# Optimization experiments

Measured on AMD Instinct MI355X. Metric: run time of the kernel, lower is better.

## Reference

```python
import jax, jax.numpy as jnp
import numpy as np

H = 256; B = 64; MAXF = 32; L = 50; S = 50
TAU = 1.0; BIAS = 0.0  # m_tau / m_bias (undefined in source; fixed constants)


def setup_inputs() -> dict:
    key = jax.random.key(0)
    ks = jax.random.split(key, 16)
    s = 1.0 / np.sqrt(H)
    return {
        "self_x": jax.random.normal(ks[0], (B, H), jnp.float32),
        "common_x": jax.random.normal(ks[1], (B, MAXF, S, H), jnp.float32),
        "common_time": jax.random.uniform(ks[2], (B, MAXF, S), jnp.float32),
        "friend_x": jax.random.normal(ks[3], (B, MAXF, L, H), jnp.float32),
        "Wih0": jax.random.normal(ks[4], (3 * H, H), jnp.float32) * s,
        "Whh0": jax.random.normal(ks[5], (3 * H, H), jnp.float32) * s,
        "bih0": jax.random.normal(ks[6], (3 * H,), jnp.float32) * s,
        "bhh0": jax.random.normal(ks[7], (3 * H,), jnp.float32) * s,
        "Wih1": jax.random.normal(ks[8], (3 * H, H), jnp.float32) * s,
        "Whh1": jax.random.normal(ks[9], (3 * H, H), jnp.float32) * s,
        "bih1": jax.random.normal(ks[10], (3 * H,), jnp.float32) * s,
        "bhh1": jax.random.normal(ks[11], (3 * H,), jnp.float32) * s,
        "Wf": jax.random.normal(ks[12], (H, 2 * H), jnp.float32) * s,   # m_linear_friend
        "Wb": jax.random.normal(ks[13], (H, H), jnp.float32) * s,       # m_linear_beta
        "friend_len": jax.random.randint(ks[14], (B, MAXF), 1, L + 1, jnp.int32),
        "friend_num": jax.random.randint(ks[15], (B,), 1, MAXF + 1, jnp.int32),
        "common_len": jax.random.randint(jax.random.fold_in(key, 99), (B, MAXF), 1, S + 1, jnp.int32),
    }


def _gru_layer(x, Wih, Whh, bih, bhh):
    # x: [N, L, H] -> outputs [N, L, H]; torch GRU gate math, zero init hidden
    def step(h, xt):
        gi = xt @ Wih.T + bih
        gh = h @ Whh.T + bhh
        ir, iz, inn = jnp.split(gi, 3, axis=-1)
        hr, hz, hn = jnp.split(gh, 3, axis=-1)
        r = jax.nn.sigmoid(ir + hr)
        z = jax.nn.sigmoid(iz + hz)
        n = jnp.tanh(inn + r * hn)
        h = (1.0 - z) * n + z * h
        return h, h
    h0 = jnp.zeros((x.shape[0], Whh.shape[1]), x.dtype)
    _, ys = jax.lax.scan(step, h0, jnp.swapaxes(x, 0, 1))
    return jnp.swapaxes(ys, 0, 1)


def reference(self_x, common_x, common_time, friend_x,
              Wih0, Whh0, bih0, bhh0, Wih1, Whh1, bih1, bhh1,
              Wf, Wb, friend_len, friend_num, common_len):
    # --- GRU over all (user, friend) sequences, flattened ---
    fx = friend_x.reshape(B * MAXF, L, H)
    fx = _gru_layer(fx, Wih0, Whh0, bih0, bhh0)
    fx = _gru_layer(fx, Wih1, Whh1, bih1, bhh1)
    fx = fx.reshape(B, MAXF, L, H)

    # mask invalid time steps, gather last valid hidden state per friend
    t_mask = (jnp.arange(L)[None, None, :] < friend_len[:, :, None])  # [B,MAXF,L]
    fx = fx * t_mask[..., None].astype(fx.dtype)
    last_idx = jnp.clip(friend_len - 1, 0, L - 1)
    friend_last = jnp.take_along_axis(fx, last_idx[:, :, None, None], axis=2)[:, :, 0, :]  # [B,MAXF,H]

    # repeat_interleave(self_x) equivalent in dense layout, concat, project
    self_rep = jnp.broadcast_to(self_x[:, None, :], (B, MAXF, H))
    sf = jnp.concatenate([self_rep, friend_last], axis=-1)  # [B,MAXF,2H]
    sf = jnp.einsum('bfk,hk->bfh', sf, Wf)                   # m_linear_friend

    # attention scores over common items: bmm + softplus
    proj_c = jnp.einsum('bfsh,gh->bfsg', common_x, Wb)       # m_linear_beta, g==H
    scores = jax.nn.softplus(jnp.einsum('bfsh,bfh->bfs', proj_c, sf))

    temporal = jnp.exp(-common_time / TAU + BIAS)
    c_mask = (jnp.arange(S)[None, None, :] < common_len[:, :, None]).astype(scores.dtype)
    tf = jnp.sum(scores * temporal * c_mask, axis=-1)        # [B,MAXF]

    # pad_sequence semantics: invalid friend slots are zero (logits and vectors)
    f_valid = (jnp.arange(MAXF)[None, :] < friend_num[:, None]).astype(tf.dtype)
    tf = tf * f_valid
    friend_last = friend_last * f_valid[..., None]

    w = jax.nn.softmax(tf, axis=-1)                          # over padded MAXF, as in source
    return jnp.sum(w[..., None] * friend_last, axis=1)       # [B,H]
```

## Files before the change

kernel.cpp:

```cpp
#include <hip/hip_runtime.h>
#include <hip/hip_bf16.h>
#include <stdint.h>

#define HD    256
#define LL    50
#define SS    50
#define NB    64
#define MAXF  32
#define NSEQ  2048
#define MB    32
#define NBLK  64
#define XP    264

typedef __attribute__((ext_vector_type(8)))  short bf16x8;
typedef __attribute__((ext_vector_type(16))) float f32x16;
typedef __attribute__((ext_vector_type(4)))  unsigned short u16x4;

__device__ __forceinline__ f32x16 mfma32(bf16x8 a, bf16x8 b, f32x16 c) {
    return __builtin_amdgcn_mfma_f32_32x32x16_bf16(a, b, c, 0, 0, 0);
}

__device__ __forceinline__ unsigned short f2bf_rne(float f) {
    union { float f; uint32_t u; } v; v.f = f;
    uint32_t u = v.u;
    uint32_t r = u + 0x7FFFu + ((u >> 16) & 1u);
    return (unsigned short)(r >> 16);
}
__device__ __forceinline__ float bf2f(unsigned short b) {
    union { float f; uint32_t u; } v; v.u = ((uint32_t)b) << 16;
    return v.f;
}

__global__ void pack_kernel(const float* __restrict__ Wih0, const float* __restrict__ Whh0,
                            const float* __restrict__ Wih1, const float* __restrict__ Whh1,
                            const float* __restrict__ Wf,
                            unsigned short* __restrict__ wpk,
                            float* __restrict__ WfT) {
    int idx = blockIdx.x * blockDim.x + threadIdx.x;
    const int TOTW = 1572864;
    if (idx < TOTW) {
        int j    = idx & 7;
        int lane = (idx >> 3) & 63;
        int fr   = (idx >> 9) % 6;
        int t2   = (idx >> 9) / 6;
        int ks   = t2 & 15;
        int m    = (t2 >> 4) & 1;
        int l    = (t2 >> 5) & 1;
        int wvv  = t2 >> 6;
        int gate = fr >> 1, plane = fr & 1;
        const float* W = (l == 0) ? (m == 0 ? Wih0 : Whh0)
                                  : (m == 0 ? Wih1 : Whh1);
        int n = gate * 256 + wvv * 32 + (lane & 31);
        int k = ks * 16 + (lane >> 5) * 8 + j;
        float v = W[n * HD + k];
        unsigned short hi = f2bf_rne(v);
        wpk[idx] = plane ? f2bf_rne(v - bf2f(hi)) : hi;
    } else {
        int idx2 = idx - TOTW;
        if (idx2 < 512 * 256) {
            int k = idx2 >> 8; int h = idx2 & 255;
            WfT[k * 256 + h] = Wf[h * 512 + k];
        }
    }
}

__global__ void sort_kernel(const int* __restrict__ flen, int* __restrict__ sid) {
    __shared__ int hist[64];
    __shared__ int offs[64];
    int tid = threadIdx.x;
    if (tid < 64) hist[tid] = 0;
    __syncthreads();
    for (int i = tid; i < NSEQ; i += blockDim.x) atomicAdd(&hist[flen[i]], 1);
    __syncthreads();
    if (tid == 0) {
        int acc = 0;
        for (int v = 1; v <= 50; v++) { offs[v] = acc; acc += hist[v]; }
    }
    __syncthreads();
    for (int i = tid; i < NSEQ; i += blockDim.x) {
        int pos = atomicAdd(&offs[flen[i]], 1);
        sid[pos] = i;
    }
}

__global__ __launch_bounds__(512, 2) __attribute__((amdgpu_waves_per_eu(2, 2)))
void gru_kernel(const float* __restrict__ friend_x,
                const int* __restrict__ flen,
                const int* __restrict__ sid,
                const unsigned short* __restrict__ wpk,
                const float* __restrict__ bih0, const float* __restrict__ bhh0,
                const float* __restrict__ bih1, const float* __restrict__ bhh1,
                float* __restrict__ friend_last) {
    __shared__ __align__(16) unsigned short Xhi[MB][XP],  Xlo[MB][XP];
    __shared__ __align__(16) unsigned short H0hi[MB][XP], H0lo[MB][XP];
    __shared__ __align__(16) unsigned short H1hi[MB][XP], H1lo[MB][XP];
    __shared__ int sidS[MB], lenS[MB];

    const int tid  = threadIdx.x;
    const int g    = blockIdx.x;
    const int wv   = tid >> 6;
    const int lane = tid & 63;
    const int l31  = lane & 31;
    const int half = lane >> 5;

    if (tid < MB) {
        int s_ = sid[g * MB + tid];
        sidS[tid] = s_;
        lenS[tid] = flen[s_];
    }
    for (int i = tid; i < MB * XP / 2; i += 512) {
        ((uint32_t*)&H0hi[0][0])[i] = 0; ((uint32_t*)&H0lo[0][0])[i] = 0;
        ((uint32_t*)&H1hi[0][0])[i] = 0; ((uint32_t*)&H1lo[0][0])[i] = 0;
    }
    __syncthreads();

    int maxlen = 0;
#pragma unroll
    for (int s = 0; s < MB; s++) maxlen = max(maxlen, lenS[s]);

    const int j0 = wv * 32 + l31;

    float b0R  = bih0[j0] + bhh0[j0];
    float b0Z  = bih0[256 + j0] + bhh0[256 + j0];
    float b0Ni = bih0[512 + j0];
    float b0Nh = bhh0[512 + j0];
    float b1R  = bih1[j0] + bhh1[j0];
    float b1Z  = bih1[256 + j0] + bhh1[256 + j0];
    float b1Ni = bih1[512 + j0];
    float b1Nh = bhh1[512 + j0];

    int srow[4];
#pragma unroll
    for (int r = 0; r < 4; r++) srow[r] = sidS[wv * 4 + r];

    const int fragBase = l31 * XP + half * 8;

    auto loadB6 = [&](bf16x8* B, const unsigned short* p) {
#pragma unroll
        for (int f = 0; f < 6; f++) B[f] = *(const bf16x8*)(p + f * 512);
    };

    auto compute9 = [&](const bf16x8* B, bf16x8 ah, bf16x8 al,
                        f32x16& aRs, f32x16& aZs, f32x16& aNs) {
        aRs = mfma32(ah, B[0], aRs);
        aZs = mfma32(ah, B[2], aZs);
        aNs = mfma32(ah, B[4], aNs);
        aRs = mfma32(al, B[0], aRs);
        aZs = mfma32(al, B[2], aZs);
        aNs = mfma32(al, B[4], aNs);
        aRs = mfma32(ah, B[1], aRs);
        aZs = mfma32(ah, B[3], aZs);
        aNs = mfma32(ah, B[5], aNs);
    };

    auto halfMM = [&](const unsigned short* pm,
                      const unsigned short* Ah_, const unsigned short* Al_,
                      f32x16& aRs, f32x16& aZs, f32x16& aNs) {
        bf16x8 B0[6], B1[6];
        loadB6(B0, pm);
        loadB6(B1, pm + 3072);
        bf16x8 ahA = *(const bf16x8*)(Ah_ + fragBase);
        bf16x8 alA = *(const bf16x8*)(Al_ + fragBase);
        bf16x8 ahB, alB;
#pragma unroll 1
        for (int ks = 0; ks < 16; ks += 2) {
            ahB = *(const bf16x8*)(Ah_ + fragBase + (ks + 1) * 16);
            alB = *(const bf16x8*)(Al_ + fragBase + (ks + 1) * 16);
            compute9(B0, ahA, alA, aRs, aZs, aNs);
            if (ks + 2 < 16) {
                loadB6(B0, pm + (size_t)(ks + 2) * 3072);
                ahA = *(const bf16x8*)(Ah_ + fragBase + (ks + 2) * 16);
                alA = *(const bf16x8*)(Al_ + fragBase + (ks + 2) * 16);
            }
            compute9(B1, ahB, alB, aRs, aZs, aNs);
            if (ks + 3 < 16) loadB6(B1, pm + (size_t)(ks + 3) * 3072);
        }
    };

    auto initAcc = [&](f32x16& a, float b) {
        f32x16 v;
#pragma unroll
        for (int i = 0; i < 16; i++) v[i] = b;
        a = v;
    };

    auto epi = [&](f32x16& aRs, f32x16& aZs, f32x16& aNis, f32x16& aNhs,
                   unsigned short (*Ohi)[XP], unsigned short (*Olo)[XP],
                   bool gather, int t) {
        const int j = j0;
#pragma unroll
        for (int rg = 0; rg < 16; rg++) {
            const int row = (rg & 3) + ((rg >> 2) << 3) + (half << 2);
            float hOld = bf2f(Ohi[row][j]) + bf2f(Olo[row][j]);
            float rr = 1.f / (1.f + __expf(-aRs[rg]));
            float zz = 1.f / (1.f + __expf(-aZs[rg]));
            float nx = aNis[rg] + rr * aNhs[rg];
            float e  = __expf(-2.f * fabsf(nx));
            float th = 1.f - 2.f * e / (1.f + e);
            th = (nx < 0.f) ? -th : th;
            float hNew = (1.f - zz) * th + zz * hOld;
            unsigned short hi_ = f2bf_rne(hNew);
            Ohi[row][j] = hi_;
            Olo[row][j] = f2bf_rne(hNew - bf2f(hi_));
            if (gather && t == lenS[row] - 1)
                friend_last[(size_t)sidS[row] * HD + j] = hNew;
        }
    };

    auto stageWrite = [&](const float4* sx) {
#pragma unroll
        for (int r = 0; r < 4; r++) {
            int row = wv * 4 + r;
            float vals[4] = { sx[r].x, sx[r].y, sx[r].z, sx[r].w };
            u16x4 hi4, lo4;
#pragma unroll
            for (int e2 = 0; e2 < 4; e2++) {
                unsigned short h_ = f2bf_rne(vals[e2]);
                hi4[e2] = h_;
                lo4[e2] = f2bf_rne(vals[e2] - bf2f(h_));
            }
            *(u16x4*)&Xhi[row][lane * 4] = hi4;
            *(u16x4*)&Xlo[row][lane * 4] = lo4;
        }
    };

    {
        float4 sx[4];
#pragma unroll
        for (int r = 0; r < 4; r++)
            sx[r] = ((const float4*)(friend_x + ((size_t)srow[r] * LL) * HD))[lane];
        stageWrite(sx);
    }
    __syncthreads();

    const unsigned short* pw0 = wpk + (size_t)(wv * 2 + 0) * 98304 + (size_t)lane * 8;
    const unsigned short* pw1 = wpk + (size_t)(wv * 2 + 1) * 98304 + (size_t)lane * 8;

#pragma unroll 1
    for (int t = 0; t < maxlen; t++) {
        int tn = (t + 1 < maxlen) ? t + 1 : t;
        float4 sx[4];
#pragma unroll
        for (int r = 0; r < 4; r++)
            sx[r] = ((const float4*)(friend_x + ((size_t)srow[r] * LL + tn) * HD))[lane];

        f32x16 aR, aZ, aNi, aNh;
        initAcc(aR, b0R); initAcc(aZ, b0Z); initAcc(aNi, b0Ni); initAcc(aNh, b0Nh);
        halfMM(pw0,         &Xhi[0][0],  &Xlo[0][0],  aR, aZ, aNi);
        halfMM(pw0 + 49152, &H0hi[0][0], &H0lo[0][0], aR, aZ, aNh);
        __syncthreads();
        epi(aR, aZ, aNi, aNh, H0hi, H0lo, false, t);
        stageWrite(sx);
        __syncthreads();
        initAcc(aR, b1R); initAcc(aZ, b1Z); initAcc(aNi, b1Ni); initAcc(aNh, b1Nh);
        halfMM(pw1,         &H0hi[0][0], &H0lo[0][0], aR, aZ, aNi);
        halfMM(pw1 + 49152, &H1hi[0][0], &H1lo[0][0], aR, aZ, aNh);
        __syncthreads();
        epi(aR, aZ, aNi, aNh, H1hi, H1lo, true, t);
    }
}

__global__ __launch_bounds__(256)
void sfv_kernel(const float* __restrict__ self_x, const float* __restrict__ fl,
                const float* __restrict__ WfT, const float* __restrict__ Wb,
                float* __restrict__ vout) {
    __shared__ float S[256];
    __shared__ float T[256][33];
    int b = blockIdx.x, tid = threadIdx.x;
    S[tid] = self_x[b * 256 + tid];
    for (int i = tid; i < 32 * 256; i += 256) {
        int f = i >> 8, k = i & 255;
        T[k][f] = fl[((size_t)(b * 32 + f)) * 256 + k];
    }
    __syncthreads();
    float acc0 = 0.f;
    for (int k = 0; k < 256; k++) acc0 += WfT[k * 256 + tid] * S[k];
    float acc[32];
#pragma unroll
    for (int f = 0; f < 32; f++) acc[f] = acc0;
    for (int k = 0; k < 256; k++) {
        float w = WfT[(256 + k) * 256 + tid];
#pragma unroll
        for (int f = 0; f < 32; f++) acc[f] += w * T[k][f];
    }
    __syncthreads();
#pragma unroll
    for (int f = 0; f < 32; f++) T[tid][f] = acc[f];
    __syncthreads();
    float av[32];
#pragma unroll
    for (int f = 0; f < 32; f++) av[f] = 0.f;
    for (int gg = 0; gg < 256; gg++) {
        float w = Wb[gg * 256 + tid];
#pragma unroll
        for (int f = 0; f < 32; f++) av[f] += w * T[gg][f];
    }
#pragma unroll
    for (int f = 0; f < 32; f++)
        vout[((size_t)(b * 32 + f)) * 256 + tid] = av[f];
}

__global__ __launch_bounds__(256)
void tf_kernel(const float* __restrict__ common_x, const float* __restrict__ common_time,
               const int* __restrict__ clen, const float* __restrict__ v,
               float* __restrict__ tf) {
    __shared__ float V[256];
    __shared__ float partial[4];
    int n = blockIdx.x, tid = threadIdx.x, wv = tid >> 6, lane = tid & 63;
    V[tid] = v[(size_t)n * 256 + tid];
    __syncthreads();
    float4 vv = ((const float4*)V)[lane];
    int cl = clen[n];
    float acc = 0.f;
    for (int s = wv; s < SS; s += 4) {
        float4 cx = ((const float4*)(common_x + ((size_t)n * SS + s) * HD))[lane];
        float d = cx.x * vv.x + cx.y * vv.y + cx.z * vv.z + cx.w * vv.w;
#pragma unroll
        for (int off = 32; off; off >>= 1) d += __shfl_xor(d, off);
        if (lane == 0 && s < cl) {
            float sp = (d > 20.f) ? d : log1pf(__expf(d));
            acc += sp * __expf(-common_time[n * SS + s]);
        }
    }
    if (lane == 0) partial[wv] = acc;
    __syncthreads();
    if (tid == 0) tf[n] = partial[0] + partial[1] + partial[2] + partial[3];
}

__global__ __launch_bounds__(256)
void out_kernel(const float* __restrict__ tf, const int* __restrict__ fnum,
                const float* __restrict__ fl, float* __restrict__ out) {
    __shared__ float e[32];
    __shared__ float tfm[32];
    __shared__ float Zs;
    int b = blockIdx.x, tid = threadIdx.x;
    int nv = fnum[b];
    if (tid < 32) tfm[tid] = (tid < nv) ? tf[b * 32 + tid] : 0.f;
    __syncthreads();
    if (tid == 0) {
        float m = tfm[0];
        for (int f = 1; f < 32; f++) m = fmaxf(m, tfm[f]);
        float Z = 0.f;
        for (int f = 0; f < 32; f++) { e[f] = __expf(tfm[f] - m); Z += e[f]; }
        Zs = Z;
    }
    __syncthreads();
    float Zi = 1.f / Zs;
    float o = 0.f;
    for (int f = 0; f < nv; f++)
        o += e[f] * Zi * fl[((size_t)(b * 32 + f)) * 256 + tid];
    out[b * 256 + tid] = o;
}

extern "C" void kernel_launch(void* const* d_in, const int* in_sizes, int n_in,
                              void* d_out, int out_size, void* d_ws, size_t ws_size,
                              hipStream_t stream) {
    (void)in_sizes; (void)n_in; (void)out_size; (void)ws_size;
    const float* self_x      = (const float*)d_in[0];
    const float* common_x    = (const float*)d_in[1];
    const float* common_time = (const float*)d_in[2];
    const float* friend_x    = (const float*)d_in[3];
    const float* Wih0 = (const float*)d_in[4];
    const float* Whh0 = (const float*)d_in[5];
    const float* bih0 = (const float*)d_in[6];
    const float* bhh0 = (const float*)d_in[7];
    const float* Wih1 = (const float*)d_in[8];
    const float* Whh1 = (const float*)d_in[9];
    const float* bih1 = (const float*)d_in[10];
    const float* bhh1 = (const float*)d_in[11];
    const float* Wf   = (const float*)d_in[12];
    const float* Wb   = (const float*)d_in[13];
    const int* flen   = (const int*)d_in[14];
    const int* fnum   = (const int*)d_in[15];
    const int* clen   = (const int*)d_in[16];
    float* out = (float*)d_out;

    char* ws = (char*)d_ws;
    unsigned short* wpk = (unsigned short*)ws; ws += (size_t)1572864 * 2;
    float* WfT = (float*)ws;  ws += (size_t)512 * 256 * 4;
    int*   sid = (int*)ws;    ws += (size_t)2048 * 4;
    float* fl  = (float*)ws;  ws += (size_t)2048 * 256 * 4;
    float* vv  = (float*)ws;  ws += (size_t)2048 * 256 * 4;
    float* tf  = (float*)ws;  ws += (size_t)2048 * 4;

    pack_kernel<<<6656, 256, 0, stream>>>(Wih0, Whh0, Wih1, Whh1, Wf, wpk, WfT);
    sort_kernel<<<1, 256, 0, stream>>>(flen, sid);
    gru_kernel<<<NBLK, 512, 0, stream>>>(friend_x, flen, sid, wpk,
                                         bih0, bhh0, bih1, bhh1, fl);
    sfv_kernel<<<64, 256, 0, stream>>>(self_x, fl, WfT, Wb, vv);
    tf_kernel<<<2048, 256, 0, stream>>>(common_x, common_time, clen, vv, tf);
    out_kernel<<<64, 256, 0, stream>>>(tf, fnum, fl, out);
}
```

Baseline: 2.524 ms.

## Precompute layer-0 input projections in a separate batched kernel before GRU recurrence

```diff
diff --git a/kernel.cpp b/kernel.cpp
--- a/kernel.cpp
+++ b/kernel.cpp
@@ -83,6 +83,104 @@
     }
 }
 
+__global__ __launch_bounds__(256) __attribute__((amdgpu_waves_per_eu(1, 1)))
+void mmih_kernel(const float* __restrict__ friend_x,
+                 const int* __restrict__ flen,
+                 const int* __restrict__ sid,
+                 const unsigned short* __restrict__ wpk,
+                 const float* __restrict__ bih0, const float* __restrict__ bhh0,
+                 float* __restrict__ Gp) {
+    __shared__ __align__(16) unsigned short XHi[4][MB][XP], XLo[4][MB][XP];
+    __shared__ int sidS[MB], lenS[MB];
+    const int tid  = threadIdx.x;
+    const int g    = blockIdx.x >> 1;
+    const int par  = blockIdx.x & 1;
+    const int wv   = tid >> 6;
+    const int lane = tid & 63;
+    const int l31  = lane & 31;
+    const int half = lane >> 5;
+
+    if (tid < MB) {
+        int s_ = sid[g * MB + tid];
+        sidS[tid] = s_;
+        lenS[tid] = flen[s_];
+    }
+    __syncthreads();
+    int maxlen = 0;
+#pragma unroll
+    for (int s = 0; s < MB; s++) maxlen = max(maxlen, lenS[s]);
+
+    const int fragBaseT = l31 * XP + half * 8;
+    float* Gbase = Gp + (size_t)g * 50 * 32 * 768;
+
+    for (int t0 = par * 4; t0 < maxlen; t0 += 8) {
+        int nt = maxlen - t0; if (nt > 4) nt = 4;
+        if (wv < nt) {
+            int tt = t0 + wv;
+            for (int r = 0; r < MB; r++) {
+                float4 v = ((const float4*)(friend_x + ((size_t)sidS[r] * LL + tt) * HD))[lane];
+                float vals[4] = { v.x, v.y, v.z, v.w };
+                u16x4 hi4, lo4;
+#pragma unroll
+                for (int e2 = 0; e2 < 4; e2++) {
+                    unsigned short h_ = f2bf_rne(vals[e2]);
+                    hi4[e2] = h_;
+                    lo4[e2] = f2bf_rne(vals[e2] - bf2f(h_));
+                }
+                *(u16x4*)&XHi[wv][r][lane * 4] = hi4;
+                *(u16x4*)&XLo[wv][r][lane * 4] = lo4;
+            }
+        }
+        __syncthreads();
+        for (int s6 = 0; s6 < 6; s6++) {
+            int s    = wv * 6 + s6;
+            int gate = s >> 3, w8 = s & 7;
+            int j    = gate * 256 + w8 * 32 + l31;
+            float bias = (gate < 2) ? (bih0[j] + bhh0[j]) : bih0[j];
+            bf16x8 BH[16], BL[16];
+            const unsigned short* pb = wpk + ((size_t)(64 * w8) * 6 + gate * 2) * 512
+                                           + (size_t)lane * 8;
+#pragma unroll
+            for (int ks = 0; ks < 16; ks++) {
+                BH[ks] = *(const bf16x8*)(pb + (size_t)ks * 3072);
+                BL[ks] = *(const bf16x8*)(pb + (size_t)ks * 3072 + 512);
+            }
+            f32x16 acc0, acc1, acc2, acc3;
+            {
+                f32x16 v;
+#pragma unroll
+                for (int i = 0; i < 16; i++) v[i] = bias;
+                acc0 = v; acc1 = v; acc2 = v; acc3 = v;
+            }
+#pragma unroll
+            for (int ks = 0; ks < 16; ks++) {
+#define MM_T(TT, ACC)                                                              \
+                if (TT < nt) {                                                     \
+                    bf16x8 ah = *(const bf16x8*)(&XHi[TT][0][0] + fragBaseT + ks * 16); \
+                    bf16x8 al = *(const bf16x8*)(&XLo[TT][0][0] + fragBaseT + ks * 16); \
+                    ACC = mfma32(ah, BH[ks], ACC);                                 \
+                    ACC = mfma32(al, BH[ks], ACC);                                 \
+                    ACC = mfma32(ah, BL[ks], ACC);                                 \
+                }
+                MM_T(0, acc0) MM_T(1, acc1) MM_T(2, acc2) MM_T(3, acc3)
+#undef MM_T
+            }
+#define ST_T(TT, ACC)                                                              \
+            if (TT < nt) {                                                         \
+                float* Gt = Gbase + (size_t)(t0 + TT) * 32 * 768;                  \
+                _Pragma("unroll")                                                  \
+                for (int rg = 0; rg < 16; rg++) {                                  \
+                    int row = (rg & 3) + ((rg >> 2) << 3) + (half << 2);           \
+                    Gt[row * 768 + j] = ACC[rg];                                   \
+                }                                                                  \
+            }
+            ST_T(0, acc0) ST_T(1, acc1) ST_T(2, acc2) ST_T(3, acc3)
+#undef ST_T
+        }
+        __syncthreads();
+    }
+}
+
 __global__ __launch_bounds__(512, 2) __attribute__((amdgpu_waves_per_eu(2, 2)))
 void gru_kernel(const float* __restrict__ friend_x,
                 const int* __restrict__ flen,
@@ -90,7 +188,8 @@
                 const unsigned short* __restrict__ wpk,
                 const float* __restrict__ bih0, const float* __restrict__ bhh0,
                 const float* __restrict__ bih1, const float* __restrict__ bhh1,
-                float* __restrict__ friend_last) {
+                float* __restrict__ friend_last,
+                const float* __restrict__ Gp, int useG) {
     __shared__ __align__(16) unsigned short Xhi[MB][XP],  Xlo[MB][XP];
     __shared__ __align__(16) unsigned short H0hi[MB][XP], H0lo[MB][XP];
     __shared__ __align__(16) unsigned short H1hi[MB][XP], H1lo[MB][XP];
@@ -224,7 +323,7 @@
         }
     };
 
-    {
+    if (!useG) {
         float4 sx[4];
 #pragma unroll
         for (int r = 0; r < 4; r++)
@@ -235,23 +334,40 @@
 
     const unsigned short* pw0 = wpk + (size_t)(wv * 2 + 0) * 98304 + (size_t)lane * 8;
     const unsigned short* pw1 = wpk + (size_t)(wv * 2 + 1) * 98304 + (size_t)lane * 8;
+    const float* Gbase = Gp + (size_t)g * 50 * 32 * 768;
 
 #pragma unroll 1
     for (int t = 0; t < maxlen; t++) {
-        int tn = (t + 1 < maxlen) ? t + 1 : t;
-        float4 sx[4];
-#pragma unroll
-        for (int r = 0; r < 4; r++)
-            sx[r] = ((const float4*)(friend_x + ((size_t)srow[r] * LL + tn) * HD))[lane];
-
         f32x16 aR, aZ, aNi, aNh;
-        initAcc(aR, b0R); initAcc(aZ, b0Z); initAcc(aNi, b0Ni); initAcc(aNh, b0Nh);
-        halfMM(pw0,         &Xhi[0][0],  &Xlo[0][0],  aR, aZ, aNi);
-        halfMM(pw0 + 49152, &H0hi[0][0], &H0lo[0][0], aR, aZ, aNh);
-        __syncthreads();
-        epi(aR, aZ, aNi, aNh, H0hi, H0lo, false, t);
-        stageWrite(sx);
-        __syncthreads();
+        if (useG) {
+            const float* Gt = Gbase + (size_t)t * 32 * 768;
+#pragma unroll
+            for (int rg = 0; rg < 16; rg++) {
+                const int row = (rg & 3) + ((rg >> 2) << 3) + (half << 2);
+                const float* gr = Gt + row * 768 + j0;
+                aR[rg]  = gr[0];
+                aZ[rg]  = gr[256];
+                aNi[rg] = gr[512];
+            }
+            initAcc(aNh, b0Nh);
+            halfMM(pw0 + 49152, &H0hi[0][0], &H0lo[0][0], aR, aZ, aNh);
+            __syncthreads();
+            epi(aR, aZ, aNi, aNh, H0hi, H0lo, false, t);
+            __syncthreads();
+        } else {
+            int tn = (t + 1 < maxlen) ? t + 1 : t;
+            float4 sx[4];
+#pragma unroll
+            for (int r = 0; r < 4; r++)
+                sx[r] = ((const float4*)(friend_x + ((size_t)srow[r] * LL + tn) * HD))[lane];
+            initAcc(aR, b0R); initAcc(aZ, b0Z); initAcc(aNi, b0Ni); initAcc(aNh, b0Nh);
+            halfMM(pw0,         &Xhi[0][0],  &Xlo[0][0],  aR, aZ, aNi);
+            halfMM(pw0 + 49152, &H0hi[0][0], &H0lo[0][0], aR, aZ, aNh);
+            __syncthreads();
+            epi(aR, aZ, aNi, aNh, H0hi, H0lo, false, t);
+            stageWrite(sx);
+            __syncthreads();
+        }
         initAcc(aR, b1R); initAcc(aZ, b1Z); initAcc(aNi, b1Ni); initAcc(aNh, b1Nh);
         halfMM(pw1,         &H0hi[0][0], &H0lo[0][0], aR, aZ, aNi);
         halfMM(pw1 + 49152, &H1hi[0][0], &H1lo[0][0], aR, aZ, aNh);
@@ -355,7 +471,7 @@
 extern "C" void kernel_launch(void* const* d_in, const int* in_sizes, int n_in,
                               void* d_out, int out_size, void* d_ws, size_t ws_size,
                               hipStream_t stream) {
-    (void)in_sizes; (void)n_in; (void)out_size; (void)ws_size;
+    (void)in_sizes; (void)n_in; (void)out_size;
     const float* self_x      = (const float*)d_in[0];
     const float* common_x    = (const float*)d_in[1];
     const float* common_time = (const float*)d_in[2];
@@ -382,11 +498,18 @@
     float* fl  = (float*)ws;  ws += (size_t)2048 * 256 * 4;
     float* vv  = (float*)ws;  ws += (size_t)2048 * 256 * 4;
     float* tf  = (float*)ws;  ws += (size_t)2048 * 4;
+    const size_t gNeed = (size_t)64 * 50 * 32 * 768 * 4;
+    size_t used = (size_t)(ws - (char*)d_ws);
+    int useG = (ws_size >= used + gNeed) ? 1 : 0;
+    float* Gp = (float*)ws;
 
     pack_kernel<<<6656, 256, 0, stream>>>(Wih0, Whh0, Wih1, Whh1, Wf, wpk, WfT);
     sort_kernel<<<1, 256, 0, stream>>>(flen, sid);
+    if (useG)
+        mmih_kernel<<<128, 256, 0, stream>>>(friend_x, flen, sid, wpk,
+                                             bih0, bhh0, Gp);
     gru_kernel<<<NBLK, 512, 0, stream>>>(friend_x, flen, sid, wpk,
-                                         bih0, bhh0, bih1, bhh1, fl);
+                                         bih0, bhh0, bih1, bhh1, fl, Gp, useG);
     sfv_kernel<<<64, 256, 0, stream>>>(self_x, fl, WfT, Wb, vv);
     tf_kernel<<<2048, 256, 0, stream>>>(common_x, common_time, clen, vv, tf);
     out_kernel<<<64, 256, 0, stream>>>(tf, fnum, fl, out);
```

Result: faster. 2.435 ms (-3.5%).
